# Optimization experiments

Hardware: AMD Instinct MI355X
Metric: run time of the kernel (lower is better)

## Reference

```python
import jax, jax.numpy as jnp
import numpy as np

B, N, DIM, H, D = 1, 1024, 512, 8, 64
BC, BS, K, W = 16, 16, 8, 256   # compress blk, selection blk, top-k blocks, sliding window
C = N // BC                     # number of compression / selection blocks
SCALE = D ** -0.5
EPS = 1e-6
NEG = -1e30


def rmsnorm(x):
    return x * jax.lax.rsqrt(jnp.mean(x * x, axis=-1, keepdims=True) + EPS)


def rope(x):  # x: [B,H,N,D], GPT-NeoX style half rotation
    half = D // 2
    inv = 1.0 / (10000.0 ** (jnp.arange(half, dtype=jnp.float32) / half))
    ang = jnp.arange(x.shape[2], dtype=jnp.float32)[:, None] * inv
    cos, sin = jnp.cos(ang), jnp.sin(ang)
    x1, x2 = x[..., :half], x[..., half:]
    return jnp.concatenate([x1 * cos - x2 * sin, x2 * cos + x1 * sin], axis=-1).astype(x.dtype)


def setup_inputs():
    key = jax.random.key(0)
    ks = jax.random.split(key, 24)
    w = lambda k, shape, fan: jax.random.normal(k, shape, jnp.float32) * (fan ** -0.5)
    return {
        'x':  jax.random.normal(ks[0], (B, N, DIM), jnp.float32),
        've': jax.random.normal(ks[1], (B, N, DIM), jnp.float32),
        'x0': jax.random.normal(ks[2], (B, N, DIM), jnp.float32),
        'lambdas': jnp.array([1.0, 0.0], jnp.float32),
        'Wq': w(ks[3], (DIM, H * D), DIM),
        'Wk': w(ks[4], (DIM, H * D), DIM),
        'Wv': w(ks[5], (DIM, H * D), DIM),
        'Wo': w(ks[6], (H * D, DIM), H * D),
        'Wg': w(ks[7], (DIM, 3 * H), DIM),
        'k_pos': w(ks[8], (H, BC, D), D),
        'v_pos': w(ks[9], (H, BC, D), D),
        'Wck': w(ks[10], (BC * D, D), BC * D),
        'bck': jnp.zeros((D,), jnp.float32),
        'Wcv': w(ks[11], (BC * D, D), BC * D),
        'bcv': jnp.zeros((D,), jnp.float32),
        'k_mem': w(ks[12], (H, 1, D), D),
        'v_mem': w(ks[13], (H, 1, D), D),
        'W1': w(ks[14], (DIM, 4 * DIM), DIM),
        'W2': w(ks[15], (4 * DIM, DIM), 4 * DIM),
    }


def _nsa_attn(xn, Wq, Wk, Wv, Wo, Wg, k_pos, v_pos, Wck, bck, Wcv, bcv, k_mem, v_mem):
    q = (xn @ Wq).reshape(B, N, H, D).transpose(0, 2, 1, 3)   # [B,H,N,D]
    k = (xn @ Wk).reshape(B, N, H, D).transpose(0, 2, 1, 3)
    v = (xn @ Wv).reshape(B, N, H, D).transpose(0, 2, 1, 3)
    q, k = rope(q), rope(k)
    i_idx = jnp.arange(N)

    # ---- compressed branch: pool kv into blocks via learned linear + intra-block pos emb ----
    kb = k.reshape(B, H, C, BC, D) + k_pos[None, :, None]
    vb = v.reshape(B, H, C, BC, D) + v_pos[None, :, None]
    ck = kb.reshape(B, H, C, BC * D) @ Wck + bck              # [B,H,C,D]
    cv = vb.reshape(B, H, C, BC * D) @ Wcv + bcv
    ckf = jnp.concatenate([jnp.broadcast_to(k_mem[None], (B, H, 1, D)), ck], axis=2)
    cvf = jnp.concatenate([jnp.broadcast_to(v_mem[None], (B, H, 1, D)), cv], axis=2)
    csim = jnp.einsum('bhid,bhjd->bhij', q, ckf) * SCALE      # [B,H,N,C+1]
    past = ((jnp.arange(C) + 1) * BC - 1)[None, :] < i_idx[:, None]   # block fully in the past
    cmask = jnp.concatenate([jnp.ones((N, 1), bool), past], axis=1)   # mem kv always visible
    cattn = jax.nn.softmax(jnp.where(cmask[None, None], csim, NEG), axis=-1)
    c_out = jnp.einsum('bhij,bhjd->bhid', cattn, cvf)

    # ---- fine selection branch: top-K blocks by compressed attention importance ----
    imp = jnp.where(past[None, None], cattn[..., 1:], NEG)    # [B,H,N,C]
    vals, sel = jax.lax.top_k(imp, K)                         # [B,H,N,K]
    valid = vals >= 0.0                                       # drop picks among masked blocks
    kb_f = k.reshape(B, H, C, BS, D)
    vb_f = v.reshape(B, H, C, BS, D)
    k_sel = jnp.take_along_axis(kb_f[:, :, None], sel[..., None, None], axis=3)  # [B,H,N,K,BS,D]
    v_sel = jnp.take_along_axis(vb_f[:, :, None], sel[..., None, None], axis=3)
    own = i_idx // BS                                         # query's own block, causal inside
    k_fine = jnp.concatenate([k_sel, kb_f[:, :, own][:, :, :, None]], axis=3)    # [B,H,N,K+1,BS,D]
    v_fine = jnp.concatenate([v_sel, vb_f[:, :, own][:, :, :, None]], axis=3)
    offs = jnp.arange(BS)
    m_sel = (sel[..., None] * BS + offs <= i_idx[None, None, :, None, None]) & valid[..., None]
    m_own = jnp.broadcast_to((own[:, None] * BS + offs <= i_idx[:, None])[None, None, :, None], (B, H, N, 1, BS))
    m_fine = jnp.concatenate([m_sel, m_own], axis=3)
    fsim = jnp.where(m_fine, jnp.einsum('bhnd,bhnksd->bhnks', q, k_fine) * SCALE, NEG)
    fattn = jax.nn.softmax(fsim.reshape(B, H, N, (K + 1) * BS), axis=-1).reshape(B, H, N, K + 1, BS)
    f_out = jnp.einsum('bhnks,bhnksd->bhnd', fattn, v_fine)

    # ---- sliding window branch ----
    smask = (i_idx[None, :] <= i_idx[:, None]) & (i_idx[:, None] - i_idx[None, :] < W)
    ssim = jnp.where(smask[None, None], jnp.einsum('bhid,bhjd->bhij', q, k) * SCALE, NEG)
    s_out = jnp.einsum('bhij,bhjd->bhid', jax.nn.softmax(ssim, axis=-1), v)

    # ---- per-head sigmoid gates combine the three strategies ----
    gates = jax.nn.sigmoid(xn @ Wg).reshape(B, N, H, 3).transpose(0, 2, 1, 3)  # [B,H,N,3]
    o = gates[..., 0:1] * c_out + gates[..., 1:2] * f_out + gates[..., 2:3] * s_out
    return o.transpose(0, 2, 1, 3).reshape(B, N, H * D) @ Wo


def reference(x, ve, x0, lambdas, Wq, Wk, Wv, Wo, Wg, k_pos, v_pos, Wck, bck, Wcv, bcv, k_mem, v_mem, W1, W2):
    # ve is accepted by NSABlock.forward but never consumed in this block
    x = lambdas[0] * x + lambdas[1] * x0
    x = x + _nsa_attn(rmsnorm(x), Wq, Wk, Wv, Wo, Wg, k_pos, v_pos, Wck, bck, Wcv, bcv, k_mem, v_mem)
    x = x + jnp.square(jax.nn.relu(rmsnorm(x) @ W1)) @ W2
    return x
```

## Files before the change

kernel.cpp:

```cpp
#include <hip/hip_runtime.h>
#include <math.h>

#define NTOK 1024
#define DIMM 512
#define NH 8
#define HD 64
#define BCB 16
#define BSB 16
#define KSEL 8
#define WWIN 256
#define CBLK 64
#define SCALE 0.125f
#define EPSV 1e-6f
#define NEGV -1e30f

typedef short bf16x8 __attribute__((ext_vector_type(8)));
typedef float f32x4 __attribute__((ext_vector_type(4)));

__device__ inline ushort f2b(float f) {
  union { float f; unsigned int u; } c; c.f = f;
  unsigned int u = c.u;
  return (ushort)((u + 0x7FFFu + ((u >> 16) & 1u)) >> 16);
}
__device__ inline float b2f(ushort h) {
// ... 195 lines not shown
  }
}

__global__ void __launch_bounds__(256)
k_gemm_w2(const ushort* __restrict__ A, const ushort* __restrict__ BT,
          float* __restrict__ outb) {
  const int Kd = 2048;
  __shared__ ushort As[64 * 40];
  __shared__ ushort Bs[64 * 40];
  int tid = threadIdx.x;
  int lane = tid & 63, w = tid >> 6;
  int rb = blockIdx.y * 64, cb = blockIdx.x * 64;
  int kb = blockIdx.z * 1024;
  int wm = (w >> 1) * 32, wn = (w & 1) * 32;
  int quad = lane >> 4, l15 = lane & 15;
  int srow = tid >> 2, scol = (tid & 3) * 8;

  f32x4 acc[2][2];
#pragma unroll
  for (int i = 0; i < 2; i++)
#pragma unroll
    for (int j = 0; j < 2; j++) acc[i][j] = (f32x4){0.f, 0.f, 0.f, 0.f};

  const ushort* ap = A  + (size_t)(rb + srow) * Kd + kb + scol;
  const ushort* bp = BT + (size_t)(cb + srow) * Kd + kb + scol;
  ushort* aw = &As[srow * 40 + scol];
  ushort* bw = &Bs[srow * 40 + scol];

  int4 pa = *(const int4*)ap;
  int4 pb = *(const int4*)bp;

  for (int k0 = 0; k0 < 1024; k0 += 32) {
    if (k0) __syncthreads();
    *(int4*)aw = pa;
    *(int4*)bw = pb;
    __syncthreads();
    if (k0 + 32 < 1024) {
      pa = *(const int4*)(ap + k0 + 32);
      pb = *(const int4*)(bp + k0 + 32);
    }
    bf16x8 af[2], bfr[2];
#pragma unroll
    for (int t = 0; t < 2; t++) {
      af[t]  = *(const bf16x8*)&As[(wm + t * 16 + l15) * 40 + quad * 8];
      bfr[t] = *(const bf16x8*)&Bs[(wn + t * 16 + l15) * 40 + quad * 8];
    }
#pragma unroll
    for (int i = 0; i < 2; i++)
#pragma unroll
      for (int j = 0; j < 2; j++)
        acc[i][j] = __builtin_amdgcn_mfma_f32_16x16x32_bf16(af[i], bfr[j],
                                                            acc[i][j], 0, 0, 0);
  }

#pragma unroll
  for (int i = 0; i < 2; i++) {
#pragma unroll
    for (int j = 0; j < 2; j++) {
      int col = cb + wn + j * 16 + l15;
#pragma unroll
      for (int r = 0; r < 4; r++) {
        int row = rb + wm + i * 16 + quad * 4 + r;
        atomicAdd(&outb[(size_t)row * 512 + col], acc[i][j][r]);
      }
    }
  }
}

__global__ void __launch_bounds__(256)
k_gemm_wo(const float* __restrict__ cg, const float* __restrict__ fg,
          const float* __restrict__ sg, const float* __restrict__ gates,
          const ushort* __restrict__ BT, float* __restrict__ P0,
          float* __restrict__ P1) {
  __shared__ ushort As[64 * 40];
  __shared__ ushort Bs[64 * 40];
  int tid = threadIdx.x;
  int lane = tid & 63, wave = tid >> 6;
  int rb = blockIdx.y * 64, cb = blockIdx.x * 64;
  int kb = blockIdx.z * 256;
  int wm = (wave >> 1) * 32, wn = (wave & 1) * 32;
  int q = lane >> 4, l15 = lane & 15;
  int srow = tid >> 2, scol = (tid & 3) * 8;

  f32x4 acc[2][2];
#pragma unroll
  for (int i = 0; i < 2; i++)
#pragma unroll
    for (int j = 0; j < 2; j++) acc[i][j] = (f32x4){0.f, 0.f, 0.f, 0.f};

  int row = rb + srow;
  const ushort* bp = BT + (size_t)(cb + srow) * 512 + kb + scol;
  ushort* aw = &As[srow * 40 + scol];
  ushort* bw = &Bs[srow * 40 + scol];

  for (int k0 = 0; k0 < 256; k0 += 32) {
    int colb = kb + k0 + scol;
    int hh = colb >> 6;
    const float* gp = gates + (size_t)row * 24 + hh * 3;
    float g0 = gp[0], g1 = gp[1], g2 = gp[2];
    size_t off = (size_t)row * 512 + colb;
    float4 c0 = *(const float4*)(cg + off), c1 = *(const float4*)(cg + off + 4);
    float4 f0 = *(const float4*)(fg + off), f1 = *(const float4*)(fg + off + 4);
    float4 s0 = *(const float4*)(sg + off), s1 = *(const float4*)(sg + off + 4);
    float va[8] = {g0 * c0.x + g1 * f0.x + g2 * s0.x,
                   g0 * c0.y + g1 * f0.y + g2 * s0.y,
                   g0 * c0.z + g1 * f0.z + g2 * s0.z,
                   g0 * c0.w + g1 * f0.w + g2 * s0.w,
                   g0 * c1.x + g1 * f1.x + g2 * s1.x,
                   g0 * c1.y + g1 * f1.y + g2 * s1.y,
                   g0 * c1.z + g1 * f1.z + g2 * s1.z,
                   g0 * c1.w + g1 * f1.w + g2 * s1.w};
    ushort h[8];
#pragma unroll
    for (int e = 0; e < 8; e++) h[e] = f2b(va[e]);
    *(int4*)aw = *(int4*)h;
    *(int4*)bw = *(const int4*)(bp + k0);
    __syncthreads();
    bf16x8 af[2], bfr[2];
#pragma unroll
    for (int t = 0; t < 2; t++) {
      af[t]  = *(const bf16x8*)&As[(wm + t * 16 + l15) * 40 + q * 8];
      bfr[t] = *(const bf16x8*)&Bs[(wn + t * 16 + l15) * 40 + q * 8];
    }
#pragma unroll
    for (int i = 0; i < 2; i++)
#pragma unroll
      for (int j = 0; j < 2; j++)
        acc[i][j] = __builtin_amdgcn_mfma_f32_16x16x32_bf16(af[i], bfr[j],
                                                            acc[i][j], 0, 0, 0);
    __syncthreads();
  }

  float* pbuf = blockIdx.z ? P1 : P0;
#pragma unroll
  for (int i = 0; i < 2; i++) {
#pragma unroll
    for (int j = 0; j < 2; j++) {
      int col = cb + wn + j * 16 + l15;
#pragma unroll
      for (int r = 0; r < 4; r++) {
        int rr = rb + wm + i * 16 + q * 4 + r;
        pbuf[(size_t)rr * 512 + col] = acc[i][j][r];
      }
    }
  }
}

__global__ void __launch_bounds__(256)
k_gemm_qkv(const ushort* __restrict__ Ah, const ushort* __restrict__ Al,
           const ushort* __restrict__ BTh, const ushort* __restrict__ BTl,
           float* __restrict__ qout, ushort* __restrict__ khm_h,
           ushort* __restrict__ khm_l, ushort* __restrict__ vhm_h,
           ushort* __restrict__ vhm_l, float* __restrict__ gates,
           const float* __restrict__ ctab, const float* __restrict__ stab,
           int Kd) {
  __shared__ ushort SM[4 * 64 * 40];
  ushort* Ash = SM;
  ushort* Asl = SM + 2560;
  ushort* Bsh = SM + 5120;
  ushort* Bsl = SM + 7680;
  int tid = threadIdx.x;
  int lane = tid & 63, wave = tid >> 6;
  int rb = blockIdx.y * 64, cb = blockIdx.x * 64;
  const bool prec = (cb < 1024);
  int wm = (wave >> 1) * 32, wn = (wave & 1) * 32;
  int q = lane >> 4, l15 = lane & 15;
  int srow = tid >> 2, scol = (tid & 3) * 8;

  f32x4 acc[2][2];
#pragma unroll
  for (int i = 0; i < 2; i++)
#pragma unroll
    for (int j = 0; j < 2; j++) acc[i][j] = (f32x4){0.f, 0.f, 0.f, 0.f};

  const ushort* aph = Ah  + (size_t)(rb + srow) * Kd + scol;
  const ushort* apl = Al  + (size_t)(rb + srow) * Kd + scol;
  const ushort* bph = BTh + (size_t)(cb + srow) * Kd + scol;
  const ushort* bpl = BTl + (size_t)(cb + srow) * Kd + scol;
  ushort* awh = &Ash[srow * 40 + scol];
  ushort* awl = &Asl[srow * 40 + scol];
  ushort* bwh = &Bsh[srow * 40 + scol];
  ushort* bwl = &Bsl[srow * 40 + scol];

  for (int k0 = 0; k0 < Kd; k0 += 32) {
    *(int4*)awh = *(const int4*)(aph + k0);
    *(int4*)bwh = *(const int4*)(bph + k0);
    if (prec) {
      *(int4*)awl = *(const int4*)(apl + k0);
      *(int4*)bwl = *(const int4*)(bpl + k0);
    }
    __syncthreads();
    bf16x8 afh[2], afl[2], bfh[2], bfl[2];
#pragma unroll
    for (int t = 0; t < 2; t++) {
      int ar = (wm + t * 16 + l15) * 40 + q * 8;
      int br = (wn + t * 16 + l15) * 40 + q * 8;
      afh[t] = *(const bf16x8*)&Ash[ar];
      bfh[t] = *(const bf16x8*)&Bsh[br];
      if (prec) {
        afl[t] = *(const bf16x8*)&Asl[ar];
        bfl[t] = *(const bf16x8*)&Bsl[br];
      }
    }
#pragma unroll
    for (int i = 0; i < 2; i++)
#pragma unroll
      for (int j = 0; j < 2; j++) {
        acc[i][j] = __builtin_amdgcn_mfma_f32_16x16x32_bf16(afh[i], bfh[j],
                                                            acc[i][j], 0, 0, 0);
        if (prec) {
          acc[i][j] = __builtin_amdgcn_mfma_f32_16x16x32_bf16(afh[i], bfl[j],
                                                              acc[i][j], 0, 0, 0);
          acc[i][j] = __builtin_amdgcn_mfma_f32_16x16x32_bf16(afl[i], bfh[j],
                                                              acc[i][j], 0, 0, 0);
        }
      }
    __syncthreads();
  }

  if (cb < 1024) {
    float* st = (float*)SM;
#pragma unroll
    for (int i = 0; i < 2; i++)
#pragma unroll
      for (int j = 0; j < 2; j++)
#pragma unroll
        for (int r = 0; r < 4; r++)
          st[(wm + i * 16 + q * 4 + r) * 66 + wn + j * 16 + l15] = acc[i][j][r];
    __syncthreads();
    int h = (cb & 511) >> 6;
#pragma unroll
    for (int e = 0; e < 8; e++) {
      int p = e * 256 + tid;
      int rw = p >> 5, d = p & 31;
      int n = rb + rw;
      float x1 = st[rw * 66 + d], x2 = st[rw * 66 + d + 32];
      float cs = ctab[n * 32 + d], sn = stab[n * 32 + d];
      float o1 = x1 * cs - x2 * sn;
      float o2 = x2 * cs + x1 * sn;
      if (cb < 512) {
        qout[(size_t)n * 512 + h * 64 + d]      = o1;
        qout[(size_t)n * 512 + h * 64 + d + 32] = o2;
      } else {
        size_t ob = (size_t)h * 65536 + (size_t)n * 64 + d;
        ushort b1 = f2b(o1), b2v = f2b(o2);
        khm_h[ob]      = b1;
        khm_h[ob + 32] = b2v;
        khm_l[ob]      = f2b(o1 - b2f(b1));
        khm_l[ob + 32] = f2b(o2 - b2f(b2v));
      }
    }
  } else {
#pragma unroll
    for (int i = 0; i < 2; i++) {
#pragma unroll
      for (int j = 0; j < 2; j++) {
        int col = cb + wn + j * 16 + l15;
#pragma unroll
        for (int r = 0; r < 4; r++) {
          int row = rb + wm + i * 16 + q * 4 + r;
          float vv = acc[i][j][r];
          if (cb >= 1536) {
            int c24 = col - 1536;
            if (c24 < 24)
              gates[(size_t)row * 24 + c24] = 1.f / (1.f + expf(-vv));
          } else {
            int c = col - 1024;
            size_t ob = (size_t)(c >> 6) * 65536 + (size_t)row * 64 + (c & 63);
            ushort hb = f2b(vv);
            vhm_h[ob] = hb;
            vhm_l[ob] = f2b(vv - b2f(hb));
          }
        }
      }
    }
  }
}

__global__ void __launch_bounds__(256)
k_mid(const ushort* __restrict__ khm_h, const ushort* __restrict__ khm_l,
      const ushort* __restrict__ vhm_h, const ushort* __restrict__ vhm_l,
      const ushort* __restrict__ WckTh, const ushort* __restrict__ WckTl,
      const ushort* __restrict__ WcvTh, const ushort* __restrict__ WcvTl,
      const float* __restrict__ pwk, const float* __restrict__ pwv,
      float* __restrict__ ckb, float* __restrict__ cvb,
      const float* __restrict__ qg, float* __restrict__ sout) {
  __shared__ union {
    struct { ushort Ash[32 * 72]; ushort Asl[32 * 72];
             ushort Bsh[64 * 72]; ushort Bsl[64 * 72]; } c;
    struct { ushort Kt[64 * 72]; ushort VT[64 * 72];
             ushort Qs[64 * 72]; ushort Ps[4][16 * 72]; } s;
  } U;
  int tid = threadIdx.x, lane = tid & 63, w = tid >> 6;
  int quad = lane >> 4, l15 = lane & 15;

  if (blockIdx.x < 32) {
    int h = blockIdx.x & 7, kv = (blockIdx.x >> 3) & 1, mh = blockIdx.x >> 4;
    const ushort* sH = kv ? vhm_h : khm_h;
    const ushort* sL = kv ? vhm_l : khm_l;
    const ushort* WTh = kv ? WcvTh : WckTh;
    const ushort* WTl = kv ? WcvTl : WckTl;
    const float* pw = (kv ? pwv : pwk) + h * 64;
    float* outp = kv ? cvb : ckb;

    ushort* Ash = U.c.Ash; ushort* Asl = U.c.Asl;
    ushort* Bsh = U.c.Bsh; ushort* Bsl = U.c.Bsl;
    int wmi = w >> 1, wnj = w & 1;
    int arow = tid >> 3, ae0 = (tid & 7) * 8;
    int brow = tid >> 2, be0 = (tid & 3) * 16;
    size_t abase = (size_t)h * 65536 + (size_t)(mh * 32 + arow) * 1024 + ae0;
    size_t bbase = (size_t)brow * 1024 + be0;

    f32x4 acc[2];
#pragma unroll
    for (int j = 0; j < 2; j++) acc[j] = (f32x4){0.f, 0.f, 0.f, 0.f};

    for (int t = 0; t < 16; t++) {
      int kb = t * 64;
      *(int4*)&Ash[arow * 72 + ae0] = *(const int4*)(sH + abase + kb);
      *(int4*)&Asl[arow * 72 + ae0] = *(const int4*)(sL + abase + kb);
      *(int4*)&Bsh[brow * 72 + be0]     = *(const int4*)(WTh + bbase + kb);
      *(int4*)&Bsh[brow * 72 + be0 + 8] = *(const int4*)(WTh + bbase + kb + 8);
      *(int4*)&Bsl[brow * 72 + be0]     = *(const int4*)(WTl + bbase + kb);
      *(int4*)&Bsl[brow * 72 + be0 + 8] = *(const int4*)(WTl + bbase + kb + 8);
      __syncthreads();
#pragma unroll
      for (int sub = 0; sub < 2; sub++) {
        int ar2 = (wmi * 16 + l15) * 72 + sub * 32 + quad * 8;
        bf16x8 afh = *(const bf16x8*)&Ash[ar2];
        bf16x8 afl = *(const bf16x8*)&Asl[ar2];
#pragma unroll
        for (int j = 0; j < 2; j++) {
          int br2 = (wnj * 32 + j * 16 + l15) * 72 + sub * 32 + quad * 8;
          bf16x8 bfh = *(const bf16x8*)&Bsh[br2];
          bf16x8 bfl = *(const bf16x8*)&Bsl[br2];
          acc[j] = __builtin_amdgcn_mfma_f32_16x16x32_bf16(afh, bfh, acc[j], 0, 0, 0);
          acc[j] = __builtin_amdgcn_mfma_f32_16x16x32_bf16(afh, bfl, acc[j], 0, 0, 0);
          acc[j] = __builtin_amdgcn_mfma_f32_16x16x32_bf16(afl, bfh, acc[j], 0, 0, 0);
        }
      }
      __syncthreads();
    }

#pragma unroll
    for (int j = 0; j < 2; j++) {
      int d = wnj * 32 + j * 16 + l15;
      float bv = pw[d];
#pragma unroll
      for (int r = 0; r < 4; r++) {
        int c = mh * 32 + wmi * 16 + quad * 4 + r;
        outp[((size_t)h * 64 + c) * 64 + d] = acc[j][r] + bv;
      }
    }
  } else {
    int sidx = blockIdx.x - 32;
    int h = sidx >> 4, i0 = (sidx & 15) * 64;
    ushort* Kt = U.s.Kt; ushort* VT = U.s.VT; ushort* Qs = U.s.Qs;

#pragma unroll
    for (int it = 0; it < 2; it++) {
      int f = it * 256 + tid;
      int r = f >> 3, d0 = (f & 7) * 8;
      const float* qp = qg + (size_t)(i0 + r) * DIMM + h * HD + d0;
      float4 t0 = *(const float4*)qp;
      float4 t1 = *(const float4*)(qp + 4);
      ushort u[8] = {f2b(t0.x), f2b(t0.y), f2b(t0.z), f2b(t0.w),
                     f2b(t1.x), f2b(t1.y), f2b(t1.z), f2b(t1.w)};
      *(int4*)&Qs[r * 72 + d0] = *(int4*)u;
    }

    int lo = i0 - (WWIN - 1); if (lo < 0) lo = 0;
    int jb_lo = lo >> 6, jb_hi = (i0 + 63) >> 6;

    float mrow[4], lrow[4];
    f32x4 Of[4];
#pragma unroll
    for (int r = 0; r < 4; r++) { mrow[r] = NEGV; lrow[r] = 0.f; }
#pragma unroll
    for (int d = 0; d < 4; d++) Of[d] = (f32x4){0.f, 0.f, 0.f, 0.f};

    for (int jb = jb_lo; jb <= jb_hi; jb++) {
      __syncthreads();
#pragma unroll
      for (int it = 0; it < 2; it++) {
        int f = it * 256 + tid;
        int r = f >> 3, c8 = (f & 7) * 8;
        const ushort* kp = khm_h + (size_t)h * 65536 + (size_t)(jb * 64 + r) * 64 + c8;
        *(int4*)&Kt[r * 72 + c8] = *(const int4*)kp;
        const ushort* vp = vhm_h + (size_t)h * 65536 + (size_t)(jb * 64 + r) * 64 + c8;
        ushort vv[8];
        *(int4*)vv = *(const int4*)vp;
#pragma unroll
        for (int e = 0; e < 8; e++) VT[(c8 + e) * 72 + r] = vv[e];
      }
      __syncthreads();

      bf16x8 qa[2];
#pragma unroll
      for (int c = 0; c < 2; c++)
        qa[c] = *(const bf16x8*)&Qs[(w * 16 + l15) * 72 + c * 32 + quad * 8];

      f32x4 sc[4];
#pragma unroll
      for (int ks = 0; ks < 4; ks++) {
        f32x4 a = (f32x4){0.f, 0.f, 0.f, 0.f};
#pragma unroll
        for (int c = 0; c < 2; c++) {
          bf16x8 kb = *(const bf16x8*)&Kt[(ks * 16 + l15) * 72 + c * 32 + quad * 8];
          a = __builtin_amdgcn_mfma_f32_16x16x32_bf16(qa[c], kb, a, 0, 0, 0);
        }
        sc[ks] = a;
      }

      float pm[4][4], rmax[4];
#pragma unroll
      for (int r = 0; r < 4; r++) rmax[r] = NEGV;
#pragma unroll
      for (int ks = 0; ks < 4; ks++) {
        int gj = jb * 64 + ks * 16 + l15;
#pragma unroll
        for (int r = 0; r < 4; r++) {
          int qi = i0 + w * 16 + quad * 4 + r;
          bool vis = (gj <= qi) && (qi - gj < WWIN);
          float s = vis ? sc[ks][r] * SCALE : NEGV;
          pm[ks][r] = s;
          rmax[r] = fmaxf(rmax[r], s);
        }
      }
#pragma unroll
      for (int off = 1; off < 16; off <<= 1)
#pragma unroll
        for (int r = 0; r < 4; r++)
          rmax[r] = fmaxf(rmax[r], __shfl_xor(rmax[r], off));

      float alpha[4], rsum[4];
#pragma unroll
      for (int r = 0; r < 4; r++) {
        float newm = fmaxf(mrow[r], rmax[r]);
        alpha[r] = expf(mrow[r] - newm);
        mrow[r] = newm;
        rsum[r] = 0.f;
      }
#pragma unroll
      for (int ks = 0; ks < 4; ks++)
#pragma unroll
        for (int r = 0; r < 4; r++) {
          float p = expf(pm[ks][r] - mrow[r]);
          pm[ks][r] = p;
          rsum[r] += p;
        }
#pragma unroll
      for (int off = 1; off < 16; off <<= 1)
#pragma unroll
        for (int r = 0; r < 4; r++)
          rsum[r] += __shfl_xor(rsum[r], off);
#pragma unroll
      for (int r = 0; r < 4; r++)
        lrow[r] = lrow[r] * alpha[r] + rsum[r];

#pragma unroll
      for (int ks = 0; ks < 4; ks++)
#pragma unroll
        for (int r = 0; r < 4; r++)
          U.s.Ps[w][(quad * 4 + r) * 72 + ks * 16 + l15] = f2b(pm[ks][r]);
#pragma unroll
      for (int d = 0; d < 4; d++)
#pragma unroll
        for (int r = 0; r < 4; r++)
          Of[d][r] *= alpha[r];

#pragma unroll
      for (int c = 0; c < 2; c++) {
        bf16x8 pa = *(const bf16x8*)&U.s.Ps[w][l15 * 72 + c * 32 + quad * 8];
#pragma unroll
        for (int d = 0; d < 4; d++) {
          bf16x8 vb = *(const bf16x8*)&VT[(d * 16 + l15) * 72 + c * 32 + quad * 8];
          Of[d] = __builtin_amdgcn_mfma_f32_16x16x32_bf16(pa, vb, Of[d], 0, 0, 0);
        }
      }
    }

#pragma unroll
    for (int d = 0; d < 4; d++)
#pragma unroll
      for (int r = 0; r < 4; r++) {
        int qi = i0 + w * 16 + quad * 4 + r;
        sout[(size_t)qi * DIMM + h * HD + d * 16 + l15] = Of[d][r] / lrow[r];
      }
  }
}

__global__ void __launch_bounds__(256)
k_cmp(const float* __restrict__ qg, const float* __restrict__ ckb,
      const float* __restrict__ cvb, const float* __restrict__ k_mem,
      const float* __restrict__ v_mem, float* __restrict__ cout,
      int* __restrict__ sel) {
  int h = blockIdx.y, i0 = blockIdx.x * 16;
  int tid = threadIdx.x, lane = tid & 63, w = tid >> 6;
  __shared__ float ckt[64][65];
  __shared__ float cvs[64][65];
  __shared__ float qs[16][64];
  __shared__ float kms[64], vms[64];
  __shared__ float sp[4][64];

#pragma unroll
  for (int r = 0; r < 4; r++) {
    int f = r * 256 + tid;
    int c = f >> 4, d0 = (f & 15) * 4;
    float4 t = *(const float4*)(ckb + ((size_t)h * 64 + c) * 64 + d0);
    ckt[d0][c] = t.x; ckt[d0 + 1][c] = t.y; ckt[d0 + 2][c] = t.z; ckt[d0 + 3][c] = t.w;
    float4 u = *(const float4*)(cvb + ((size_t)h * 64 + c) * 64 + d0);
    cvs[c][d0] = u.x; cvs[c][d0 + 1] = u.y; cvs[c][d0 + 2] = u.z; cvs[c][d0 + 3] = u.w;
  }
  {
    int r = tid >> 4, d0 = (tid & 15) * 4;
    float4 t = *(const float4*)(qg + (size_t)(i0 + r) * DIMM + h * HD + d0);
    qs[r][d0] = t.x; qs[r][d0 + 1] = t.y; qs[r][d0 + 2] = t.z; qs[r][d0 + 3] = t.w;
  }
  if (tid < 64) kms[tid] = k_mem[h * HD + tid];
  else if (tid < 128) vms[tid - 64] = v_mem[h * HD + tid - 64];
  __syncthreads();

  for (int s = 0; s < 4; s++) {
    int ql = w * 4 + s, qi = i0 + ql;
    float dot = 0.f, dm = 0.f;
#pragma unroll 8
    for (int e = 0; e < 64; e++) {
      float qe = qs[ql][e];
      dot = fmaf(qe, ckt[e][lane], dot);
      dm  = fmaf(qe, kms[e], dm);
    }
    bool vis = (lane * BCB + BCB - 1) < qi;
    float sj = vis ? dot * SCALE : NEGV;
    float smem = dm * SCALE;
    float m = wred_max(fmaxf(sj, smem));
    float p = expf(sj - m);
    float pmem = expf(smem - m);
    float l = wred_sum(p) + pmem;
    float inv = 1.f / l;

    float impv = vis ? p : NEGV;
#pragma unroll
    for (int kk = 0; kk < KSEL; kk++) {
      float bv = impv; int bi = lane;
#pragma unroll
      for (int off = 32; off > 0; off >>= 1) {
        float ov = __shfl_xor(bv, off);
        int   oi = __shfl_xor(bi, off);
        if (ov > bv || (ov == bv && oi < bi)) { bv = ov; bi = oi; }
      }
      if (lane == 0) sel[((size_t)h * NTOK + qi) * KSEL + kk] = (bv >= 0.f) ? bi : -1;
      if (lane == bi) impv = NEGV;
    }

    sp[w][lane] = p;
    float od = pmem * vms[lane];
#pragma unroll 8
    for (int j = 0; j < 64; j++) od = fmaf(sp[w][j], cvs[j][lane], od);
    cout[(size_t)qi * DIMM + h * HD + lane] = od * inv;
  }
}

__global__ void __launch_bounds__(256)
k_fine(const float* __restrict__ qg, const ushort* __restrict__ khm_bf,
       const ushort* __restrict__ vhm_bf, const int* __restrict__ sel,
       float* __restrict__ fout) {
  int i = blockIdx.x, h = blockIdx.y;
  int tid = threadIdx.x, lane = tid & 63, w = tid >> 6;
  __shared__ float qsh[64];
  __shared__ ushort vsb[144 * 64];
  __shared__ float sp[144];
  __shared__ int selS[8];
  __shared__ float mred[4], sredS[4];
  __shared__ float pacc[4][64];

  int own = i >> 4;
  if (tid < 64) qsh[tid] = qg[(size_t)i * DIMM + h * HD + tid];
  if (tid >= 64 && tid < 72)
    selS[tid - 64] = sel[((size_t)h * NTOK + i) * KSEL + tid - 64];
  __syncthreads();

  const ushort* kbase = khm_bf + (size_t)h * 65536;
  const ushort* vbase = vhm_bf + (size_t)h * 65536;

#pragma unroll
  for (int it = 0; it < 5; it++) {
    int idx = it * 256 + tid;
    if (idx < 1152) {
      int row = idx >> 3, c8 = (idx & 7) * 8;
      int kk = row >> 4;
      int bidx = (kk < KSEL) ? selS[kk] : own;
      if (bidx < 0) bidx = 0;
      *(int4*)&vsb[row * 64 + c8] =
          *(const int4*)(vbase + (size_t)(bidx * BSB + (row & 15)) * 64 + c8);
    }
  }

  float s_loc = NEGV;
  bool active = (tid < 144);
  if (active) {
    int kk = tid >> 4;
    int bidx; bool vis;
    if (kk < KSEL) {
      bidx = selS[kk];
      vis = (bidx >= 0);
      if (!vis) bidx = 0;
    } else {
      bidx = own;
      vis = (tid - 128) <= (i & 15);
    }
    const ushort* kr = kbase + (size_t)(bidx * BSB + (tid & 15)) * 64;
    float dot = 0.f;
#pragma unroll
    for (int e8 = 0; e8 < 8; e8++) {
      ushort kv[8];
      *(int4*)kv = *(const int4*)(kr + e8 * 8);
#pragma unroll
      for (int e = 0; e < 8; e++)
        dot = fmaf(qsh[e8 * 8 + e], b2f(kv[e]), dot);
    }
    s_loc = vis ? dot * SCALE : NEGV;
  }
  float mw = wred_max(s_loc);
  if (lane == 0) mred[w] = mw;
  __syncthreads();
  float m = fmaxf(fmaxf(mred[0], mred[1]), fmaxf(mred[2], mred[3]));
  float p = active ? expf(s_loc - m) : 0.f;
  float sw = wred_sum(p);
  if (lane == 0) sredS[w] = sw;
  if (active) sp[tid] = p;
  __syncthreads();
  float l = sredS[0] + sredS[1] + sredS[2] + sredS[3];

  float acc = 0.f;
  int j0 = w * 36;
#pragma unroll 6
  for (int jj = 0; jj < 36; jj++) {
    int j = j0 + jj;
    acc = fmaf(sp[j], b2f(vsb[j * 64 + lane]), acc);
  }
  pacc[w][lane] = acc;
  __syncthreads();
  if (w == 0)
    fout[(size_t)i * DIMM + h * HD + lane] =
        (pacc[0][lane] + pacc[1][lane] + pacc[2][lane] + pacc[3][lane]) / l;
}

extern "C" void kernel_launch(void* const* d_in, const int* in_sizes, int n_in,
                              void* d_out, int out_size, void* d_ws, size_t ws_size,
                              hipStream_t stream) {
  const float* x     = (const float*)d_in[0];
  const float* ve    = (const float*)d_in[1]; (void)ve;
  const float* x0    = (const float*)d_in[2];
  const float* lam   = (const float*)d_in[3];
  const float* Wq    = (const float*)d_in[4];
  const float* Wk    = (const float*)d_in[5];
  const float* Wv    = (const float*)d_in[6];
  const float* Wo    = (const float*)d_in[7];
  const float* Wg    = (const float*)d_in[8];
  const float* k_pos = (const float*)d_in[9];
  const float* v_pos = (const float*)d_in[10];
  const float* Wck   = (const float*)d_in[11];
  const float* bck   = (const float*)d_in[12];
  const float* Wcv   = (const float*)d_in[13];
  const float* bcv   = (const float*)d_in[14];
  const float* k_mem = (const float*)d_in[15];
  const float* v_mem = (const float*)d_in[16];
  const float* W1    = (const float*)d_in[17];
  const float* W2    = (const float*)d_in[18];
  float* out = (float*)d_out;
  float* ws  = (float*)d_ws;

  const size_t NW = (size_t)NTOK * DIMM;
  float* xr    = ws;
  float* xn    = ws + 1 * NW;
  float* q     = ws + 2 * NW;
  float* kslot = ws + 3 * NW;
  float* vslot = ws + 4 * NW;
  float* coutb = ws + 5 * NW;
  float* foutb = ws + 6 * NW;
  float* soutb = ws + 7 * NW;
  float* gates = ws + 9 * NW;
  float* ckb   = gates + 32768;
  float* cvb   = ckb + 32768;
  int*   selb  = (int*)(cvb + 32768);
  ushort* qkvTh = (ushort*)(cvb + 32768 + 65536);
  ushort* qkvTl = qkvTh + 1600 * 512;
  ushort* WoT   = qkvTl + 1600 * 512;
  ushort* W1T   = WoT   + 512 * 512;
  ushort* W2T   = W1T   + 2048 * 512;
  ushort* WckTh = W2T   + 512 * 2048;
  ushort* WckTl = WckTh + 64 * 1024;
  ushort* WcvTh = WckTl + 64 * 1024;
  ushort* WcvTl = WcvTh + 64 * 1024;
  float* ctab   = (float*)(WcvTl + 64 * 1024);
  float* stab   = ctab + 32768;
  float* pwk    = stab + 32768;
  float* pwv    = pwk + 512;

  ushort* xnh = (ushort*)xn;
  ushort* xnl = xnh + NW;
  ushort* khm_h = (ushort*)kslot;
  ushort* khm_l = khm_h + 524288;
  ushort* vhm_h = (ushort*)vslot;
  ushort* vhm_l = vhm_h + 524288;
  float* p0w = kslot;
  float* p1w = q;
  ushort* ybf = (ushort*)soutb;
  ushort* h1b = (ushort*)q;

  WtrPack pk;
  pk.d[0] = {Wq, qkvTh,              qkvTl,              512, 512,  512};
  pk.d[1] = {Wk, qkvTh + 512 * 512,  qkvTl + 512 * 512,  512, 512,  512};
  pk.d[2] = {Wv, qkvTh + 1024 * 512, qkvTl + 1024 * 512, 512, 512,  512};
  pk.d[3] = {Wo, WoT, nullptr,  512, 512,  512};
  pk.d[4] = {W1, W1T, nullptr,  512, 2048, 2048};
  pk.d[5] = {W2, W2T, nullptr, 2048, 512,  512};
  pk.d[6] = {Wck, WckTh, WckTl, 1024, 64, 64};
  pk.d[7] = {Wcv, WcvTh, WcvTl, 1024, 64, 64};
  pk.d[8] = {Wg, qkvTh + 1536 * 512, qkvTl + 1536 * 512, 512, 24, 64};
  int cum = 0;
  for (int e = 0; e < 9; e++) {
    cum += (pk.d[e].Npad / 32) * (pk.d[e].K / 32);
    pk.cum[e] = cum;
  }

  k_pre<<<cum + NTOK + 128 + 16, 256, 0, stream>>>(
      pk, x, x0, lam, xr, xnh, xnl, ctab, stab,
      k_pos, v_pos, Wck, Wcv, bck, bcv, pwk, pwv);

  k_gemm_qkv<<<dim3(25, NTOK / 64), 256, 0, stream>>>(
      xnh, xnl, qkvTh, qkvTl, q, khm_h, khm_l, vhm_h, vhm_l, gates,
      ctab, stab, 512);

  k_mid<<<160, 256, 0, stream>>>(khm_h, khm_l, vhm_h, vhm_l,
                                 WckTh, WckTl, WcvTh, WcvTl,
                                 pwk, pwv, ckb, cvb, q, soutb);

  k_cmp<<<dim3(NTOK / 16, NH), 256, 0, stream>>>(q, ckb, cvb, k_mem, v_mem,
                                                 coutb, selb);
  k_fine<<<dim3(NTOK, NH), 256, 0, stream>>>(q, khm_h, vhm_h, selb, foutb);

  k_gemm_wo<<<dim3(512 / 64, NTOK / 64, 2), 256, 0, stream>>>(
      coutb, foutb, soutb, gates, WoT, p0w, p1w);
  k_rms_bf<<<NTOK, 256, 0, stream>>>(xr, p0w, p1w, out, ybf);

  k_gemm_w1<<<dim3(2048 / 64, NTOK / 128), 256, 0, stream>>>(ybf, W1T, h1b);
  k_gemm_w2<<<dim3(512 / 64, NTOK / 64, 2), 256, 0, stream>>>(h1b, W2T, out);
}
```

Baseline: 250.8 us.

## Regroup mid kernels: split compression GEMM, fuse sliding-window with compressed attention

The compression GEMM (ck/cv) now runs as its own 32-block kernel. The sliding-window attention and compressed-attention/top-k selection are merged into one 640-block launch sharing a shared-memory union. Previously the tiny GEMM shared a launch with sliding-window attention, and the compressed branch needed a separate launch that waited on it. Now the independent sliding-window work sits in the same launch as the compressed branch. This keeps the launch count the same but aims to fill the GPU better, and s_setprio hints are added around the MFMA sections. The cost is that the small 32-block GEMM launch runs alone and serializes before everything else.

```diff
diff --git a/kernel.cpp b/kernel.cpp
--- a/kernel.cpp
+++ b/kernel.cpp
@@ -497,82 +497,90 @@
 }
 
 __global__ void __launch_bounds__(256)
-k_mid(const ushort* __restrict__ khm_h, const ushort* __restrict__ khm_l,
-      const ushort* __restrict__ vhm_h, const ushort* __restrict__ vhm_l,
-      const ushort* __restrict__ WckTh, const ushort* __restrict__ WckTl,
-      const ushort* __restrict__ WcvTh, const ushort* __restrict__ WcvTl,
-      const float* __restrict__ pwk, const float* __restrict__ pwv,
-      float* __restrict__ ckb, float* __restrict__ cvb,
-      const float* __restrict__ qg, float* __restrict__ sout) {
+k_ckcv(const ushort* __restrict__ khm_h, const ushort* __restrict__ khm_l,
+       const ushort* __restrict__ vhm_h, const ushort* __restrict__ vhm_l,
+       const ushort* __restrict__ WckTh, const ushort* __restrict__ WckTl,
+       const ushort* __restrict__ WcvTh, const ushort* __restrict__ WcvTl,
+       const float* __restrict__ pwk, const float* __restrict__ pwv,
+       float* __restrict__ ckb, float* __restrict__ cvb) {
+  __shared__ ushort Ash[32 * 72], Asl[32 * 72];
+  __shared__ ushort Bsh[64 * 72], Bsl[64 * 72];
+  int tid = threadIdx.x, lane = tid & 63, w = tid >> 6;
+  int quad = lane >> 4, l15 = lane & 15;
+  int h = blockIdx.x & 7, kv = (blockIdx.x >> 3) & 1, mh = blockIdx.x >> 4;
+  const ushort* sH = kv ? vhm_h : khm_h;
+  const ushort* sL = kv ? vhm_l : khm_l;
+  const ushort* WTh = kv ? WcvTh : WckTh;
+  const ushort* WTl = kv ? WcvTl : WckTl;
+  const float* pw = (kv ? pwv : pwk) + h * 64;
+  float* outp = kv ? cvb : ckb;
+
+  int wmi = w >> 1, wnj = w & 1;
+  int arow = tid >> 3, ae0 = (tid & 7) * 8;
+  int brow = tid >> 2, be0 = (tid & 3) * 16;
+  size_t abase = (size_t)h * 65536 + (size_t)(mh * 32 + arow) * 1024 + ae0;
+  size_t bbase = (size_t)brow * 1024 + be0;
+
+  f32x4 acc[2];
+#pragma unroll
+  for (int j = 0; j < 2; j++) acc[j] = (f32x4){0.f, 0.f, 0.f, 0.f};
+
+  for (int t = 0; t < 16; t++) {
+    int kb = t * 64;
+    *(int4*)&Ash[arow * 72 + ae0] = *(const int4*)(sH + abase + kb);
+    *(int4*)&Asl[arow * 72 + ae0] = *(const int4*)(sL + abase + kb);
+    *(int4*)&Bsh[brow * 72 + be0]     = *(const int4*)(WTh + bbase + kb);
+    *(int4*)&Bsh[brow * 72 + be0 + 8] = *(const int4*)(WTh + bbase + kb + 8);
+    *(int4*)&Bsl[brow * 72 + be0]     = *(const int4*)(WTl + bbase + kb);
+    *(int4*)&Bsl[brow * 72 + be0 + 8] = *(const int4*)(WTl + bbase + kb + 8);
+    __syncthreads();
+#pragma unroll
+    for (int sub = 0; sub < 2; sub++) {
+      int ar2 = (wmi * 16 + l15) * 72 + sub * 32 + quad * 8;
+      bf16x8 afh = *(const bf16x8*)&Ash[ar2];
+      bf16x8 afl = *(const bf16x8*)&Asl[ar2];
+#pragma unroll
+      for (int j = 0; j < 2; j++) {
+        int br2 = (wnj * 32 + j * 16 + l15) * 72 + sub * 32 + quad * 8;
+        bf16x8 bfh = *(const bf16x8*)&Bsh[br2];
+        bf16x8 bfl = *(const bf16x8*)&Bsl[br2];
+        acc[j] = __builtin_amdgcn_mfma_f32_16x16x32_bf16(afh, bfh, acc[j], 0, 0, 0);
+        acc[j] = __builtin_amdgcn_mfma_f32_16x16x32_bf16(afh, bfl, acc[j], 0, 0, 0);
+        acc[j] = __builtin_amdgcn_mfma_f32_16x16x32_bf16(afl, bfh, acc[j], 0, 0, 0);
+      }
+    }
+    __syncthreads();
+  }
+
+#pragma unroll
+  for (int j = 0; j < 2; j++) {
+    int d = wnj * 32 + j * 16 + l15;
+    float bv = pw[d];
+#pragma unroll
+    for (int r = 0; r < 4; r++) {
+      int c = mh * 32 + wmi * 16 + quad * 4 + r;
+      outp[((size_t)h * 64 + c) * 64 + d] = acc[j][r] + bv;
+    }
+  }
+}
+
+__global__ void __launch_bounds__(256)
+k_sc(const float* __restrict__ qg, const ushort* __restrict__ khm_h,
+     const ushort* __restrict__ vhm_h, float* __restrict__ sout,
+     const float* __restrict__ ckb, const float* __restrict__ cvb,
+     const float* __restrict__ k_mem, const float* __restrict__ v_mem,
+     float* __restrict__ cout, int* __restrict__ sel) {
   __shared__ union {
-    struct { ushort Ash[32 * 72]; ushort Asl[32 * 72];
-             ushort Bsh[64 * 72]; ushort Bsl[64 * 72]; } c;
     struct { ushort Kt[64 * 72]; ushort VT[64 * 72];
              ushort Qs[64 * 72]; ushort Ps[4][16 * 72]; } s;
+    struct { float ckt[64][65]; float cvs[64][65]; float qs[16][64];
+             float kms[64]; float vms[64]; float sp[4][64]; } c;
   } U;
   int tid = threadIdx.x, lane = tid & 63, w = tid >> 6;
   int quad = lane >> 4, l15 = lane & 15;
 
-  if (blockIdx.x < 32) {
-    int h = blockIdx.x & 7, kv = (blockIdx.x >> 3) & 1, mh = blockIdx.x >> 4;
-    const ushort* sH = kv ? vhm_h : khm_h;
-    const ushort* sL = kv ? vhm_l : khm_l;
-    const ushort* WTh = kv ? WcvTh : WckTh;
-    const ushort* WTl = kv ? WcvTl : WckTl;
-    const float* pw = (kv ? pwv : pwk) + h * 64;
-    float* outp = kv ? cvb : ckb;
-
-    ushort* Ash = U.c.Ash; ushort* Asl = U.c.Asl;
-    ushort* Bsh = U.c.Bsh; ushort* Bsl = U.c.Bsl;
-    int wmi = w >> 1, wnj = w & 1;
-    int arow = tid >> 3, ae0 = (tid & 7) * 8;
-    int brow = tid >> 2, be0 = (tid & 3) * 16;
-    size_t abase = (size_t)h * 65536 + (size_t)(mh * 32 + arow) * 1024 + ae0;
-    size_t bbase = (size_t)brow * 1024 + be0;
-
-    f32x4 acc[2];
-#pragma unroll
-    for (int j = 0; j < 2; j++) acc[j] = (f32x4){0.f, 0.f, 0.f, 0.f};
-
-    for (int t = 0; t < 16; t++) {
-      int kb = t * 64;
-      *(int4*)&Ash[arow * 72 + ae0] = *(const int4*)(sH + abase + kb);
-      *(int4*)&Asl[arow * 72 + ae0] = *(const int4*)(sL + abase + kb);
-      *(int4*)&Bsh[brow * 72 + be0]     = *(const int4*)(WTh + bbase + kb);
-      *(int4*)&Bsh[brow * 72 + be0 + 8] = *(const int4*)(WTh + bbase + kb + 8);
-      *(int4*)&Bsl[brow * 72 + be0]     = *(const int4*)(WTl + bbase + kb);
-      *(int4*)&Bsl[brow * 72 + be0 + 8] = *(const int4*)(WTl + bbase + kb + 8);
-      __syncthreads();
-#pragma unroll
-      for (int sub = 0; sub < 2; sub++) {
-        int ar2 = (wmi * 16 + l15) * 72 + sub * 32 + quad * 8;
-        bf16x8 afh = *(const bf16x8*)&Ash[ar2];
-        bf16x8 afl = *(const bf16x8*)&Asl[ar2];
-#pragma unroll
-        for (int j = 0; j < 2; j++) {
-          int br2 = (wnj * 32 + j * 16 + l15) * 72 + sub * 32 + quad * 8;
-          bf16x8 bfh = *(const bf16x8*)&Bsh[br2];
-          bf16x8 bfl = *(const bf16x8*)&Bsl[br2];
-          acc[j] = __builtin_amdgcn_mfma_f32_16x16x32_bf16(afh, bfh, acc[j], 0, 0, 0);
-          acc[j] = __builtin_amdgcn_mfma_f32_16x16x32_bf16(afh, bfl, acc[j], 0, 0, 0);
-          acc[j] = __builtin_amdgcn_mfma_f32_16x16x32_bf16(afl, bfh, acc[j], 0, 0, 0);
-        }
-      }
-      __syncthreads();
-    }
-
-#pragma unroll
-    for (int j = 0; j < 2; j++) {
-      int d = wnj * 32 + j * 16 + l15;
-      float bv = pw[d];
-#pragma unroll
-      for (int r = 0; r < 4; r++) {
-        int c = mh * 32 + wmi * 16 + quad * 4 + r;
-        outp[((size_t)h * 64 + c) * 64 + d] = acc[j][r] + bv;
-      }
-    }
-  } else {
-    int sidx = blockIdx.x - 32;
+  if (blockIdx.x < 128) {
+    int sidx = blockIdx.x;
     int h = sidx >> 4, i0 = (sidx & 15) * 64;
     ushort* Kt = U.s.Kt; ushort* VT = U.s.VT; ushort* Qs = U.s.Qs;
 
@@ -620,6 +628,7 @@
         qa[c] = *(const bf16x8*)&Qs[(w * 16 + l15) * 72 + c * 32 + quad * 8];
 
       f32x4 sc[4];
+      __builtin_amdgcn_s_setprio(1);
 #pragma unroll
       for (int ks = 0; ks < 4; ks++) {
         f32x4 a = (f32x4){0.f, 0.f, 0.f, 0.f};
@@ -630,6 +639,7 @@
         }
         sc[ks] = a;
       }
+      __builtin_amdgcn_s_setprio(0);
 
       float pm[4][4], rmax[4];
 #pragma unroll
@@ -688,6 +698,7 @@
         for (int r = 0; r < 4; r++)
           Of[d][r] *= alpha[r];
 
+      __builtin_amdgcn_s_setprio(1);
 #pragma unroll
       for (int c = 0; c < 2; c++) {
         bf16x8 pa = *(const bf16x8*)&U.s.Ps[w][l15 * 72 + c * 32 + quad * 8];
@@ -697,6 +708,7 @@
           Of[d] = __builtin_amdgcn_mfma_f32_16x16x32_bf16(pa, vb, Of[d], 0, 0, 0);
         }
       }
+      __builtin_amdgcn_s_setprio(0);
     }
 
 #pragma unroll
@@ -706,77 +718,69 @@
         int qi = i0 + w * 16 + quad * 4 + r;
         sout[(size_t)qi * DIMM + h * HD + d * 16 + l15] = Of[d][r] / lrow[r];
       }
-  }
-}
-
-__global__ void __launch_bounds__(256)
-k_cmp(const float* __restrict__ qg, const float* __restrict__ ckb,
-      const float* __restrict__ cvb, const float* __restrict__ k_mem,
-      const float* __restrict__ v_mem, float* __restrict__ cout,
-      int* __restrict__ sel) {
-  int h = blockIdx.y, i0 = blockIdx.x * 16;
-  int tid = threadIdx.x, lane = tid & 63, w = tid >> 6;
-  __shared__ float ckt[64][65];
-  __shared__ float cvs[64][65];
-  __shared__ float qs[16][64];
-  __shared__ float kms[64], vms[64];
-  __shared__ float sp[4][64];
-
-#pragma unroll
-  for (int r = 0; r < 4; r++) {
-    int f = r * 256 + tid;
-    int c = f >> 4, d0 = (f & 15) * 4;
-    float4 t = *(const float4*)(ckb + ((size_t)h * 64 + c) * 64 + d0);
-    ckt[d0][c] = t.x; ckt[d0 + 1][c] = t.y; ckt[d0 + 2][c] = t.z; ckt[d0 + 3][c] = t.w;
-    float4 u = *(const float4*)(cvb + ((size_t)h * 64 + c) * 64 + d0);
-    cvs[c][d0] = u.x; cvs[c][d0 + 1] = u.y; cvs[c][d0 + 2] = u.z; cvs[c][d0 + 3] = u.w;
-  }
-  {
-    int r = tid >> 4, d0 = (tid & 15) * 4;
-    float4 t = *(const float4*)(qg + (size_t)(i0 + r) * DIMM + h * HD + d0);
-    qs[r][d0] = t.x; qs[r][d0 + 1] = t.y; qs[r][d0 + 2] = t.z; qs[r][d0 + 3] = t.w;
-  }
-  if (tid < 64) kms[tid] = k_mem[h * HD + tid];
-  else if (tid < 128) vms[tid - 64] = v_mem[h * HD + tid - 64];
-  __syncthreads();
-
-  for (int s = 0; s < 4; s++) {
-    int ql = w * 4 + s, qi = i0 + ql;
-    float dot = 0.f, dm = 0.f;
+  } else {
+    int idx = blockIdx.x - 128;
+    int h = idx >> 6, i0 = (idx & 63) * 16;
+
+#pragma unroll
+    for (int r = 0; r < 4; r++) {
+      int f = r * 256 + tid;
+      int c = f >> 4, d0 = (f & 15) * 4;
+      float4 t = *(const float4*)(ckb + ((size_t)h * 64 + c) * 64 + d0);
+      U.c.ckt[d0][c] = t.x; U.c.ckt[d0 + 1][c] = t.y;
+      U.c.ckt[d0 + 2][c] = t.z; U.c.ckt[d0 + 3][c] = t.w;
+      float4 u = *(const float4*)(cvb + ((size_t)h * 64 + c) * 64 + d0);
+      U.c.cvs[c][d0] = u.x; U.c.cvs[c][d0 + 1] = u.y;
+      U.c.cvs[c][d0 + 2] = u.z; U.c.cvs[c][d0 + 3] = u.w;
+    }
+    {
+      int r = tid >> 4, d0 = (tid & 15) * 4;
+      float4 t = *(const float4*)(qg + (size_t)(i0 + r) * DIMM + h * HD + d0);
+      U.c.qs[r][d0] = t.x; U.c.qs[r][d0 + 1] = t.y;
+      U.c.qs[r][d0 + 2] = t.z; U.c.qs[r][d0 + 3] = t.w;
+    }
+    if (tid < 64) U.c.kms[tid] = k_mem[h * HD + tid];
+    else if (tid < 128) U.c.vms[tid - 64] = v_mem[h * HD + tid - 64];
+    __syncthreads();
+
+    for (int s = 0; s < 4; s++) {
+      int ql = w * 4 + s, qi = i0 + ql;
+      float dot = 0.f, dm = 0.f;
 #pragma unroll 8
-    for (int e = 0; e < 64; e++) {
-      float qe = qs[ql][e];
-      dot = fmaf(qe, ckt[e][lane], dot);
-      dm  = fmaf(qe, kms[e], dm);
-    }
-    bool vis = (lane * BCB + BCB - 1) < qi;
-    float sj = vis ? dot * SCALE : NEGV;
-    float smem = dm * SCALE;
-    float m = wred_max(fmaxf(sj, smem));
-    float p = expf(sj - m);
-    float pmem = expf(smem - m);
-    float l = wred_sum(p) + pmem;
-    float inv = 1.f / l;
-
-    float impv = vis ? p : NEGV;
-#pragma unroll
-    for (int kk = 0; kk < KSEL; kk++) {
-      float bv = impv; int bi = lane;
-#pragma unroll
-      for (int off = 32; off > 0; off >>= 1) {
-        float ov = __shfl_xor(bv, off);
-        int   oi = __shfl_xor(bi, off);
-        if (ov > bv || (ov == bv && oi < bi)) { bv = ov; bi = oi; }
-      }
-      if (lane == 0) sel[((size_t)h * NTOK + qi) * KSEL + kk] = (bv >= 0.f) ? bi : -1;
-      if (lane == bi) impv = NEGV;
-    }
-
-    sp[w][lane] = p;
-    float od = pmem * vms[lane];
+      for (int e = 0; e < 64; e++) {
+        float qe = U.c.qs[ql][e];
+        dot = fmaf(qe, U.c.ckt[e][lane], dot);
+        dm  = fmaf(qe, U.c.kms[e], dm);
+      }
+      bool vis = (lane * BCB + BCB - 1) < qi;
+      float sj = vis ? dot * SCALE : NEGV;
+      float smem = dm * SCALE;
+      float m = wred_max(fmaxf(sj, smem));
+      float p = expf(sj - m);
+      float pmem = expf(smem - m);
+      float l = wred_sum(p) + pmem;
+      float inv = 1.f / l;
+
+      float impv = vis ? p : NEGV;
+#pragma unroll
+      for (int kk = 0; kk < KSEL; kk++) {
+        float bv = impv; int bi = lane;
+#pragma unroll
+        for (int off = 32; off > 0; off >>= 1) {
+          float ov = __shfl_xor(bv, off);
+          int   oi = __shfl_xor(bi, off);
+          if (ov > bv || (ov == bv && oi < bi)) { bv = ov; bi = oi; }
+        }
+        if (lane == 0) sel[((size_t)h * NTOK + qi) * KSEL + kk] = (bv >= 0.f) ? bi : -1;
+        if (lane == bi) impv = NEGV;
+      }
+
+      U.c.sp[w][lane] = p;
+      float od = pmem * U.c.vms[lane];
 #pragma unroll 8
-    for (int j = 0; j < 64; j++) od = fmaf(sp[w][j], cvs[j][lane], od);
-    cout[(size_t)qi * DIMM + h * HD + lane] = od * inv;
+      for (int j = 0; j < 64; j++) od = fmaf(U.c.sp[w][j], U.c.cvs[j][lane], od);
+      cout[(size_t)qi * DIMM + h * HD + lane] = od * inv;
+    }
   }
 }
 
@@ -952,12 +956,13 @@
       xnh, xnl, qkvTh, qkvTl, q, khm_h, khm_l, vhm_h, vhm_l, gates,
       ctab, stab, 512);
 
-  k_mid<<<160, 256, 0, stream>>>(khm_h, khm_l, vhm_h, vhm_l,
+  k_ckcv<<<32, 256, 0, stream>>>(khm_h, khm_l, vhm_h, vhm_l,
                                  WckTh, WckTl, WcvTh, WcvTl,
-                                 pwk, pwv, ckb, cvb, q, soutb);
-
-  k_cmp<<<dim3(NTOK / 16, NH), 256, 0, stream>>>(q, ckb, cvb, k_mem, v_mem,
-                                                 coutb, selb);
+                                 pwk, pwv, ckb, cvb);
+
+  k_sc<<<640, 256, 0, stream>>>(q, khm_h, vhm_h, soutb,
+                                ckb, cvb, k_mem, v_mem, coutb, selb);
+
   k_fine<<<dim3(NTOK, NH), 256, 0, stream>>>(q, khm_h, vhm_h, selb, foutb);
 
   k_gemm_wo<<<dim3(512 / 64, NTOK / 64, 2), 256, 0, stream>>>(
```

After: 255.7 us. Within noise of the previous version (+2.0%).

## Enlarge QKV GEMM tile to 128 rows with register prefetch; add MFMA priority hints

Applied to the files above, without the earlier changes.

The QKV projection GEMM now computes 128x64 tiles instead of 64x64. The next K-slice is prefetched into registers while the current slice is consumed from shared memory, and the two barriers per iteration are reordered accordingly. The RoPE epilogue is split into two 64-row halves so the existing staging buffer can be reused. Separately, s_setprio hints are placed around the MFMA sections of the sliding-window attention kernel. Together these aim to hide global-load latency and raise data reuse, at the cost of a smaller grid (200 blocks), more registers and more LDS.

```diff
diff --git a/kernel.cpp b/kernel.cpp
--- a/kernel.cpp
+++ b/kernel.cpp
@@ -371,58 +371,83 @@
            float* __restrict__ qout, ushort* __restrict__ khm_h,
            ushort* __restrict__ khm_l, ushort* __restrict__ vhm_h,
            ushort* __restrict__ vhm_l, float* __restrict__ gates,
-           const float* __restrict__ ctab, const float* __restrict__ stab,
-           int Kd) {
-  __shared__ ushort SM[4 * 64 * 40];
+           const float* __restrict__ ctab, const float* __restrict__ stab) {
+  const int Kd = 512;
+  __shared__ ushort SM[15360];
   ushort* Ash = SM;
-  ushort* Asl = SM + 2560;
-  ushort* Bsh = SM + 5120;
-  ushort* Bsl = SM + 7680;
+  ushort* Asl = SM + 5120;
+  ushort* Bsh = SM + 10240;
+  ushort* Bsl = SM + 12800;
   int tid = threadIdx.x;
   int lane = tid & 63, wave = tid >> 6;
-  int rb = blockIdx.y * 64, cb = blockIdx.x * 64;
+  int rb = blockIdx.y * 128, cb = blockIdx.x * 64;
   const bool prec = (cb < 1024);
-  int wm = (wave >> 1) * 32, wn = (wave & 1) * 32;
+  int wm = (wave >> 1) * 64, wn = (wave & 1) * 32;
   int q = lane >> 4, l15 = lane & 15;
-  int srow = tid >> 2, scol = (tid & 3) * 8;
-
-  f32x4 acc[2][2];
-#pragma unroll
-  for (int i = 0; i < 2; i++)
+  int srA = tid >> 1, scA = (tid & 1) * 16;
+  int srB = tid >> 2, scB = (tid & 3) * 8;
+
+  f32x4 acc[4][2];
+#pragma unroll
+  for (int i = 0; i < 4; i++)
 #pragma unroll
     for (int j = 0; j < 2; j++) acc[i][j] = (f32x4){0.f, 0.f, 0.f, 0.f};
 
-  const ushort* aph = Ah  + (size_t)(rb + srow) * Kd + scol;
-  const ushort* apl = Al  + (size_t)(rb + srow) * Kd + scol;
-  const ushort* bph = BTh + (size_t)(cb + srow) * Kd + scol;
-  const ushort* bpl = BTl + (size_t)(cb + srow) * Kd + scol;
-  ushort* awh = &Ash[srow * 40 + scol];
-  ushort* awl = &Asl[srow * 40 + scol];
-  ushort* bwh = &Bsh[srow * 40 + scol];
-  ushort* bwl = &Bsl[srow * 40 + scol];
+  const ushort* aph = Ah  + (size_t)(rb + srA) * Kd + scA;
+  const ushort* apl = Al  + (size_t)(rb + srA) * Kd + scA;
+  const ushort* bph = BTh + (size_t)(cb + srB) * Kd + scB;
+  const ushort* bpl = BTl + (size_t)(cb + srB) * Kd + scB;
+  ushort* awh = &Ash[srA * 40 + scA];
+  ushort* awl = &Asl[srA * 40 + scA];
+  ushort* bwh = &Bsh[srB * 40 + scB];
+  ushort* bwl = &Bsl[srB * 40 + scB];
+
+  int4 ph0 = *(const int4*)aph;
+  int4 ph1 = *(const int4*)(aph + 8);
+  int4 pbh = *(const int4*)bph;
+  int4 pl0, pl1, pbl;
+  if (prec) {
+    pl0 = *(const int4*)apl;
+    pl1 = *(const int4*)(apl + 8);
+    pbl = *(const int4*)bpl;
+  }
 
   for (int k0 = 0; k0 < Kd; k0 += 32) {
-    *(int4*)awh = *(const int4*)(aph + k0);
-    *(int4*)bwh = *(const int4*)(bph + k0);
+    if (k0) __syncthreads();
+    *(int4*)awh = ph0; *(int4*)(awh + 8) = ph1;
+    *(int4*)bwh = pbh;
     if (prec) {
-      *(int4*)awl = *(const int4*)(apl + k0);
-      *(int4*)bwl = *(const int4*)(bpl + k0);
+      *(int4*)awl = pl0; *(int4*)(awl + 8) = pl1;
+      *(int4*)bwl = pbl;
     }
     __syncthreads();
-    bf16x8 afh[2], afl[2], bfh[2], bfl[2];
-#pragma unroll
-    for (int t = 0; t < 2; t++) {
-      int ar = (wm + t * 16 + l15) * 40 + q * 8;
-      int br = (wn + t * 16 + l15) * 40 + q * 8;
-      afh[t] = *(const bf16x8*)&Ash[ar];
-      bfh[t] = *(const bf16x8*)&Bsh[br];
+    if (k0 + 32 < Kd) {
+      ph0 = *(const int4*)(aph + k0 + 32);
+      ph1 = *(const int4*)(aph + k0 + 40);
+      pbh = *(const int4*)(bph + k0 + 32);
       if (prec) {
-        afl[t] = *(const bf16x8*)&Asl[ar];
-        bfl[t] = *(const bf16x8*)&Bsl[br];
-      }
-    }
-#pragma unroll
-    for (int i = 0; i < 2; i++)
+        pl0 = *(const int4*)(apl + k0 + 32);
+        pl1 = *(const int4*)(apl + k0 + 40);
+        pbl = *(const int4*)(bpl + k0 + 32);
+      }
+    }
+    bf16x8 afh[4], bfh[2], afl[4], bfl[2];
+#pragma unroll
+    for (int t = 0; t < 4; t++)
+      afh[t] = *(const bf16x8*)&Ash[(wm + t * 16 + l15) * 40 + q * 8];
+#pragma unroll
+    for (int t = 0; t < 2; t++)
+      bfh[t] = *(const bf16x8*)&Bsh[(wn + t * 16 + l15) * 40 + q * 8];
+    if (prec) {
+#pragma unroll
+      for (int t = 0; t < 4; t++)
+        afl[t] = *(const bf16x8*)&Asl[(wm + t * 16 + l15) * 40 + q * 8];
+#pragma unroll
+      for (int t = 0; t < 2; t++)
+        bfl[t] = *(const bf16x8*)&Bsl[(wn + t * 16 + l15) * 40 + q * 8];
+    }
+#pragma unroll
+    for (int i = 0; i < 4; i++)
 #pragma unroll
       for (int j = 0; j < 2; j++) {
         acc[i][j] = __builtin_amdgcn_mfma_f32_16x16x32_bf16(afh[i], bfh[j],
@@ -434,44 +459,49 @@
                                                               acc[i][j], 0, 0, 0);
         }
       }
-    __syncthreads();
-  }
-
-  if (cb < 1024) {
+  }
+
+  if (prec) {
     float* st = (float*)SM;
-#pragma unroll
-    for (int i = 0; i < 2; i++)
-#pragma unroll
-      for (int j = 0; j < 2; j++)
-#pragma unroll
-        for (int r = 0; r < 4; r++)
-          st[(wm + i * 16 + q * 4 + r) * 66 + wn + j * 16 + l15] = acc[i][j][r];
-    __syncthreads();
     int h = (cb & 511) >> 6;
 #pragma unroll
-    for (int e = 0; e < 8; e++) {
-      int p = e * 256 + tid;
-      int rw = p >> 5, d = p & 31;
-      int n = rb + rw;
-      float x1 = st[rw * 66 + d], x2 = st[rw * 66 + d + 32];
-      float cs = ctab[n * 32 + d], sn = stab[n * 32 + d];
-      float o1 = x1 * cs - x2 * sn;
-      float o2 = x2 * cs + x1 * sn;
-      if (cb < 512) {
-        qout[(size_t)n * 512 + h * 64 + d]      = o1;
-        qout[(size_t)n * 512 + h * 64 + d + 32] = o2;
-      } else {
-        size_t ob = (size_t)h * 65536 + (size_t)n * 64 + d;
-        ushort b1 = f2b(o1), b2v = f2b(o2);
-        khm_h[ob]      = b1;
-        khm_h[ob + 32] = b2v;
-        khm_l[ob]      = f2b(o1 - b2f(b1));
-        khm_l[ob + 32] = f2b(o2 - b2f(b2v));
+    for (int hb = 0; hb < 2; hb++) {
+      __syncthreads();
+      if ((wave >> 1) == hb) {
+#pragma unroll
+        for (int i = 0; i < 4; i++)
+#pragma unroll
+          for (int j = 0; j < 2; j++)
+#pragma unroll
+            for (int r = 0; r < 4; r++)
+              st[(i * 16 + q * 4 + r) * 66 + wn + j * 16 + l15] = acc[i][j][r];
+      }
+      __syncthreads();
+#pragma unroll
+      for (int e = 0; e < 8; e++) {
+        int p = e * 256 + tid;
+        int rw = p >> 5, d = p & 31;
+        int n = rb + hb * 64 + rw;
+        float x1 = st[rw * 66 + d], x2 = st[rw * 66 + d + 32];
+        float cs = ctab[n * 32 + d], sn = stab[n * 32 + d];
+        float o1 = x1 * cs - x2 * sn;
+        float o2 = x2 * cs + x1 * sn;
+        if (cb < 512) {
+          qout[(size_t)n * 512 + h * 64 + d]      = o1;
+          qout[(size_t)n * 512 + h * 64 + d + 32] = o2;
+        } else {
+          size_t ob = (size_t)h * 65536 + (size_t)n * 64 + d;
+          ushort b1 = f2b(o1), b2v = f2b(o2);
+          khm_h[ob]      = b1;
+          khm_h[ob + 32] = b2v;
+          khm_l[ob]      = f2b(o1 - b2f(b1));
+          khm_l[ob + 32] = f2b(o2 - b2f(b2v));
+        }
       }
     }
   } else {
 #pragma unroll
-    for (int i = 0; i < 2; i++) {
+    for (int i = 0; i < 4; i++) {
 #pragma unroll
       for (int j = 0; j < 2; j++) {
         int col = cb + wn + j * 16 + l15;
@@ -620,6 +650,7 @@
         qa[c] = *(const bf16x8*)&Qs[(w * 16 + l15) * 72 + c * 32 + quad * 8];
 
       f32x4 sc[4];
+      __builtin_amdgcn_s_setprio(1);
 #pragma unroll
       for (int ks = 0; ks < 4; ks++) {
         f32x4 a = (f32x4){0.f, 0.f, 0.f, 0.f};
@@ -630,6 +661,7 @@
         }
         sc[ks] = a;
       }
+      __builtin_amdgcn_s_setprio(0);
 
       float pm[4][4], rmax[4];
 #pragma unroll
@@ -688,6 +720,7 @@
         for (int r = 0; r < 4; r++)
           Of[d][r] *= alpha[r];
 
+      __builtin_amdgcn_s_setprio(1);
 #pragma unroll
       for (int c = 0; c < 2; c++) {
         bf16x8 pa = *(const bf16x8*)&U.s.Ps[w][l15 * 72 + c * 32 + quad * 8];
@@ -697,6 +730,7 @@
           Of[d] = __builtin_amdgcn_mfma_f32_16x16x32_bf16(pa, vb, Of[d], 0, 0, 0);
         }
       }
+      __builtin_amdgcn_s_setprio(0);
     }
 
 #pragma unroll
@@ -948,9 +982,9 @@
       pk, x, x0, lam, xr, xnh, xnl, ctab, stab,
       k_pos, v_pos, Wck, Wcv, bck, bcv, pwk, pwv);
 
-  k_gemm_qkv<<<dim3(25, NTOK / 64), 256, 0, stream>>>(
+  k_gemm_qkv<<<dim3(25, NTOK / 128), 256, 0, stream>>>(
       xnh, xnl, qkvTh, qkvTl, q, khm_h, khm_l, vhm_h, vhm_l, gates,
-      ctab, stab, 512);
+      ctab, stab);
 
   k_mid<<<160, 256, 0, stream>>>(khm_h, khm_l, vhm_h, vhm_l,
                                  WckTh, WckTl, WcvTh, WcvTl,
@@ -958,6 +992,7 @@
 
   k_cmp<<<dim3(NTOK / 16, NH), 256, 0, stream>>>(q, ckb, cvb, k_mem, v_mem,
                                                  coutb, selb);
+
   k_fine<<<dim3(NTOK, NH), 256, 0, stream>>>(q, khm_h, vhm_h, selb, foutb);
 
   k_gemm_wo<<<dim3(512 / 64, NTOK / 64, 2), 256, 0, stream>>>(
```

After: 251.2 us. About the same (+0.2%).
